# Performance work log

Measured on AMD Instinct MI355X. Metric: run time of the kernel, lower is better.

The kernel has to match this reference:

```python
import jax, jax.numpy as jnp
import numpy as np

N_HEAD = 16
N_EMBD = 1024
B, T = 2, 2048


def setup_inputs() -> dict:
    key = jax.random.key(0)
    ks = jax.random.split(key, 5)
    C = N_EMBD
    x = jax.random.normal(ks[0], (B, T, C), dtype=jnp.float32)
    # nn.Linear default init scale ~ 1/sqrt(fan_in); use small normal for numerics
    s = 1.0 / np.sqrt(C)
    W_attn = jax.random.normal(ks[1], (C, 3 * C), dtype=jnp.float32) * s
    b_attn = jax.random.normal(ks[2], (3 * C,), dtype=jnp.float32) * s
    W_proj = jax.random.normal(ks[3], (C, C), dtype=jnp.float32) * s
    b_proj = jax.random.normal(ks[4], (C,), dtype=jnp.float32) * s
    return {"x": x, "W_attn": W_attn, "b_attn": b_attn, "W_proj": W_proj, "b_proj": b_proj}


def reference(x, W_attn, b_attn, W_proj, b_proj):
    Bs, Ts, C = x.shape
    H = N_HEAD
    D = C // H  # head dim
    qkv = x @ W_attn + b_attn  # [B, T, 3C]
    q, k, v = jnp.split(qkv, 3, axis=2)
    # [B, T, H, D] -> [B, H, T, D]
    q = q.reshape(Bs, Ts, H, D).transpose(0, 2, 1, 3)
    k = k.reshape(Bs, Ts, H, D).transpose(0, 2, 1, 3)
    v = v.reshape(Bs, Ts, H, D).transpose(0, 2, 1, 3)
    scale = 1.0 / jnp.sqrt(jnp.asarray(D, dtype=x.dtype))
    att = jnp.einsum("bhqd,bhkd->bhqk", q, k) * scale  # [B, H, T, T]
    causal = jnp.tril(jnp.ones((Ts, Ts), dtype=bool))
    att = jnp.where(causal, att, -jnp.inf)
    att = jax.nn.softmax(att, axis=-1)
    y = jnp.einsum("bhqk,bhkd->bhqd", att, v)  # [B, H, T, D]
    y = y.transpose(0, 2, 1, 3).reshape(Bs, Ts, C)
    return y @ W_proj + b_proj
```

## Files before the change

kernel.cpp:

```cpp
#include <hip/hip_runtime.h>
#include <stdint.h>

typedef unsigned short u16;
typedef __attribute__((ext_vector_type(8))) short bf16x8;
typedef __attribute__((ext_vector_type(4))) float f32x4;
typedef __attribute__((ext_vector_type(4))) int   i32x4;
typedef __attribute__((ext_vector_type(4))) unsigned int u32x4;
typedef __attribute__((ext_vector_type(4))) unsigned short u16x4;

#define MFMA16(a, b, c) __builtin_amdgcn_mfma_f32_16x16x32_bf16((a), (b), (c), 0, 0, 0)

#define BATCH 2
#define TSEQ  2048
#define CEMB  1024
#define NHEAD 16
#define DHEAD 64
#define BHTOT 32
#define MROWS 4096

__device__ __forceinline__ u16 bf16r(float f) {
  uint32_t u = __builtin_bit_cast(uint32_t, f);
  u += 0x7fffu + ((u >> 16) & 1u);
  return (u16)(u >> 16);
}

__device__ __forceinline__ uint32_t cvt_pk_bf16(float lo, float hi) {
  uint32_t r;
  asm("v_cvt_pk_bf16_f32 %0, %1, %2" : "=v"(r) : "v"(lo), "v"(hi));
  return r;
}

__device__ __forceinline__ float bf2f(short v) {
  return __builtin_bit_cast(float, ((uint32_t)(u16)v) << 16);
}

__device__ __forceinline__ bf16x8 scale8(bf16x8 a, float s) {
  bf16x8 r;
#pragma unroll
  for (int i = 0; i < 8; i++) r[i] = (short)bf16r(bf2f(a[i]) * s);
  return r;
}

__device__ __forceinline__ void gl2lds16(const void* g, void* l) {
  __builtin_amdgcn_global_load_lds(
      (const __attribute__((address_space(1))) uint32_t*)g,
      (__attribute__((address_space(3))) uint32_t*)l, 16, 0, 0);
}

__global__ void prep(const float* __restrict__ x, u16* __restrict__ xb,
                     const float* __restrict__ W_attn, u16* __restrict__ WaT,
                     const float* __restrict__ W_proj, u16* __restrict__ WpT) {
  __shared__ float t[32][33];
  const int bid = blockIdx.x;
  if (bid < 4096) {
    int i = (bid * 256 + threadIdx.x) * 4;
    f32x4 v = *(const f32x4*)(x + i);
    u16x4 o;
    o[0] = bf16r(v[0]); o[1] = bf16r(v[1]); o[2] = bf16r(v[2]); o[3] = bf16r(v[3]);
    *(u16x4*)(xb + i) = o;
    return;
  }
  const float* W; u16* WT; int K, N, idx;
  if (bid < 7168) { W = W_attn; WT = WaT; K = 1024; N = 3072; idx = bid - 4096;
                    idx = (idx % 96) | ((idx / 96) << 16); }
  else            { W = W_proj; WT = WpT; K = 1024; N = 1024; idx = bid - 7168;
                    idx = (idx % 32) | ((idx / 32) << 16); }
  int n0 = (idx & 0xffff) * 32, k0 = (idx >> 16) * 32;
  int tx = threadIdx.x & 31, ty = threadIdx.x >> 5;
  for (int i = 0; i < 4; i++)
    t[ty + i * 8][tx] = W[(size_t)(k0 + ty + i * 8) * N + n0 + tx];
  __syncthreads();
  for (int i = 0; i < 4; i++)
    WT[(size_t)(n0 + ty + i * 8) * K + k0 + tx] = bf16r(t[tx][ty + i * 8]);
}

__device__ __forceinline__ void gemm_mainloop(const u16* __restrict__ A,
                                              const u16* __restrict__ Bt,
                                              int K, int m0, int n0,
                                              u16* AsU, u16* BsU, f32x4 acc[4][4]) {
  const int tid = threadIdx.x;
  const int wv = tid >> 6, ln = tid & 63;
  const int lr = ln & 15, lg = ln >> 4;
  const int wr = (wv >> 1) * 64, wc = (wv & 1) * 64;

  for (int mi = 0; mi < 4; mi++)
    for (int ni = 0; ni < 4; ni++) acc[mi][ni] = f32x4{0.f, 0.f, 0.f, 0.f};

  for (int k0 = 0; k0 < K; k0 += 32) {
    for (int p = 0; p < 2; ++p) {
      int chunk = p * 256 + tid;
      int row = chunk >> 2;
      int c8  = (chunk & 3) << 3;
      u16* abase = AsU + (size_t)(p * 256 + wv * 64) * 8;
      u16* bbase = BsU + (size_t)(p * 256 + wv * 64) * 8;
      gl2lds16(A  + (size_t)(m0 + row) * K + k0 + c8, abase);
      gl2lds16(Bt + (size_t)(n0 + row) * K + k0 + c8, bbase);
    }
    __syncthreads();
    bf16x8 af[4], bf[4];
    for (int mi = 0; mi < 4; mi++)
      af[mi] = *(const bf16x8*)&AsU[(size_t)(wr + mi * 16 + lr) * 32 + lg * 8];
    for (int ni = 0; ni < 4; ni++)
      bf[ni] = *(const bf16x8*)&BsU[(size_t)(wc + ni * 16 + lr) * 32 + lg * 8];
    for (int mi = 0; mi < 4; mi++)
      for (int ni = 0; ni < 4; ni++)
        acc[mi][ni] = MFMA16(af[mi], bf[ni], acc[mi][ni]);
    __syncthreads();
  }
}

__global__ __launch_bounds__(256, 2) void qkv_gemm(const u16* __restrict__ xb,
                                                   const u16* __restrict__ WaT,
                                                   const float* __restrict__ b_attn,
                                                   u16* __restrict__ qb, u16* __restrict__ kb,
                                                   u16* __restrict__ vT) {
  __shared__ u16 AsU[128 * 32];
  __shared__ u16 BsU[128 * 32];
  const int m0 = blockIdx.y * 128, n0 = blockIdx.x * 128;
  f32x4 acc[4][4];
  gemm_mainloop(xb, WaT, CEMB, m0, n0, AsU, BsU, acc);

  const int tid = threadIdx.x;
  const int wv = tid >> 6, ln = tid & 63, lr = ln & 15, lg = ln >> 4;
  const int wr = (wv >> 1) * 64, wc = (wv & 1) * 64;
  for (int mi = 0; mi < 4; mi++)
    for (int ni = 0; ni < 4; ni++) {
      int col = n0 + wc + ni * 16 + lr;
      float bias = b_attn[col];
      int which = col >> 10;
      int cl = col & 1023, h = cl >> 6, d = cl & 63;
      for (int j = 0; j < 4; j++) {
        int m = m0 + wr + mi * 16 + lg * 4 + j;
        int b = m >> 11, t = m & 2047;
        u16 bv = bf16r(acc[mi][ni][j] + bias);
        size_t bh = (size_t)(b * NHEAD + h);
        if (which == 0)      qb[(bh * TSEQ + t) * DHEAD + d] = bv;
        else if (which == 1) kb[(bh * TSEQ + t) * DHEAD + d] = bv;
        else                 vT[(bh * DHEAD + d) * TSEQ + t] = bv;
      }
    }
}

__global__ __launch_bounds__(256, 4) void attn(const u16* __restrict__ qb,
                                               const u16* __restrict__ kb,
                                               const u16* __restrict__ vT,
                                               u16* __restrict__ yb) {
  const int flat = blockIdx.x;
  const int x = flat & 7;
  const int l = flat >> 3;
  const int r = l & 31, a = l >> 5, rq = r & 7;
  const int bh = 4 * x + (r >> 3);
  const int qblk = (a == 0) ? 31 - rq : (a == 1) ? rq : (a == 2) ? 23 - rq : 8 + rq;

  const int tid = threadIdx.x, wv = tid >> 6, ln = tid & 63, lr = ln & 15, lg = ln >> 4;
  const int b1 = lg >> 1, b0 = lg & 1;

  __shared__ u16 Ks[2][64][72];
  __shared__ u16 Vs[2][64][72];

  const int wq0 = qblk * 64 + wv * 16;
  const float SCL = 0.125f * 1.44269504f;

  bf16x8 qf0, qf1;
  {
    const u16* qrow = qb + ((size_t)bh * TSEQ + (wq0 + lr)) * DHEAD + lg * 8;
    qf0 = scale8(*(const bf16x8*)(qrow), SCL);
    qf1 = scale8(*(const bf16x8*)(qrow + 32), SCL);
  }

  f32x4 acc[4];
#pragma unroll
  for (int df = 0; df < 4; df++) acc[df] = f32x4{0.f, 0.f, 0.f, 0.f};
  float mrun = -1e30f, lrun = 0.f;

  const int ntiles = qblk + 1;
  const int srow = tid >> 3, sc8 = (tid & 7) << 3;

  i32x4 kreg[2], vreg[2];
#pragma unroll
  for (int p = 0; p < 2; p++) {
    int row = p * 32 + srow;
    *(i32x4*)&Ks[0][row][sc8] = *(const i32x4*)(kb + ((size_t)bh * TSEQ + row) * DHEAD + sc8);
    *(i32x4*)&Vs[0][row][sc8] = *(const i32x4*)(vT + ((size_t)bh * DHEAD + row) * TSEQ + sc8);
  }
#pragma unroll
  for (int p = 0; p < 2; p++) {
    int row = p * 32 + srow;
    kreg[p] = *(const i32x4*)(kb + ((size_t)bh * TSEQ + 64 + row) * DHEAD + sc8);
    vreg[p] = *(const i32x4*)(vT + ((size_t)bh * DHEAD + row) * TSEQ + 64 + sc8);
  }

  int c = 0;
  for (int kt = 0; kt < ntiles; kt++) {
    const int kbase = kt * 64;
    __syncthreads();

    f32x4 s[4];
#pragma unroll
    for (int st = 0; st < 4; st++) {
      bf16x8 kf0 = *(const bf16x8*)&Ks[c][st * 16 + lr][lg * 8];
      bf16x8 kf1 = *(const bf16x8*)&Ks[c][st * 16 + lr][32 + lg * 8];
      f32x4 z = f32x4{0.f, 0.f, 0.f, 0.f};
      z = MFMA16(kf0, qf0, z);
      z = MFMA16(kf1, qf1, z);
      s[st] = z;
    }

    if (kt + 1 < ntiles) {
#pragma unroll
      for (int p = 0; p < 2; p++) {
        int row = p * 32 + srow;
        *(i32x4*)&Ks[c ^ 1][row][sc8] = kreg[p];
        *(i32x4*)&Vs[c ^ 1][row][sc8] = vreg[p];
      }
    }
    if (kt + 2 < ntiles) {
      const int nb = kbase + 128;
#pragma unroll
      for (int p = 0; p < 2; p++) {
        int row = p * 32 + srow;
        kreg[p] = *(const i32x4*)(kb + ((size_t)bh * TSEQ + nb + row) * DHEAD + sc8);
        vreg[p] = *(const i32x4*)(vT + ((size_t)bh * DHEAD + row) * TSEQ + nb + sc8);
      }
    }

    float mt = -1e30f;
    if (kt == ntiles - 1) {
      const int qg = wq0 + lr;
#pragma unroll
      for (int st = 0; st < 4; st++)
#pragma unroll
        for (int j = 0; j < 4; j++) {
          int kg = kbase + st * 16 + lg * 4 + j;
          float v = (kg <= qg) ? s[st][j] : -1e30f;
          s[st][j] = v;
          mt = fmaxf(mt, v);
        }
    } else {
#pragma unroll
      for (int st = 0; st < 4; st++)
#pragma unroll
        for (int j = 0; j < 4; j++) mt = fmaxf(mt, s[st][j]);
    }
    mt = fmaxf(mt, __shfl_xor(mt, 16));
    mt = fmaxf(mt, __shfl_xor(mt, 32));
    if (!__all(mt <= mrun)) {
      float mnew = fmaxf(mrun, mt);
      float al = __builtin_amdgcn_exp2f(mrun - mnew);
#pragma unroll
      for (int df = 0; df < 4; df++)
#pragma unroll
        for (int j = 0; j < 4; j++) acc[df][j] *= al;
      lrun *= al;
      mrun = mnew;
    }
    float rs = 0.f;
#pragma unroll
    for (int st = 0; st < 4; st++)
#pragma unroll
      for (int j = 0; j < 4; j++) {
        float p = __builtin_amdgcn_exp2f(s[st][j] - mrun);
        s[st][j] = p;
        rs += p;
      }
    rs += __shfl_xor(rs, 16);
    rs += __shfl_xor(rs, 32);
    lrun += rs;

    uint32_t W[4][2];
#pragma unroll
    for (int st = 0; st < 4; st++) {
      W[st][0] = cvt_pk_bf16(s[st][0], s[st][1]);
      W[st][1] = cvt_pk_bf16(s[st][2], s[st][3]);
    }
    uint32_t Ka[2], Kb[2], Xa[2], Xb[2];
#pragma unroll
    for (int h = 0; h < 2; h++) {
      uint32_t S1a = b1 ? W[0][h] : W[1][h];
      uint32_t S1b = b1 ? W[2][h] : W[3][h];
      Xa[h] = __shfl_xor(S1a, 32);
      Xb[h] = __shfl_xor(S1b, 32);
      Ka[h] = b1 ? W[1][h] : W[0][h];
      Kb[h] = b1 ? W[3][h] : W[2][h];
    }
    const bool e = (b0 == b1);
    uint32_t Ta[2], Tb[2], Ra[2], Rb[2];
#pragma unroll
    for (int h = 0; h < 2; h++) {
      uint32_t Cah = e ? Xa[h] : Ka[h];
      uint32_t Cbh = e ? Xb[h] : Kb[h];
      Ta[h] = e ? Ka[h] : Xa[h];
      Tb[h] = e ? Kb[h] : Xb[h];
      Ra[h] = __shfl_xor(Cah, 16);
      Rb[h] = __shfl_xor(Cbh, 16);
    }
    u32x4 w0, w1;
    w0[0] = b0 ? Ra[0] : Ta[0];  w0[1] = b0 ? Ra[1] : Ta[1];
    w0[2] = b0 ? Ta[0] : Ra[0];  w0[3] = b0 ? Ta[1] : Ra[1];
    w1[0] = b0 ? Rb[0] : Tb[0];  w1[1] = b0 ? Rb[1] : Tb[1];
    w1[2] = b0 ? Tb[0] : Rb[0];  w1[3] = b0 ? Tb[1] : Rb[1];
    bf16x8 pf0 = __builtin_bit_cast(bf16x8, w0);
    bf16x8 pf1 = __builtin_bit_cast(bf16x8, w1);

#pragma unroll
    for (int df = 0; df < 4; df++) {
      bf16x8 vf0 = *(const bf16x8*)&Vs[c][df * 16 + lr][lg * 8];
      bf16x8 vf1 = *(const bf16x8*)&Vs[c][df * 16 + lr][32 + lg * 8];
      acc[df] = MFMA16(vf0, pf0, acc[df]);
      acc[df] = MFMA16(vf1, pf1, acc[df]);
    }
    c ^= 1;
  }

  const int b = bh >> 4, h = bh & 15;
  float inv = 1.f / lrun;
  int tg = wq0 + lr;
#pragma unroll
  for (int df = 0; df < 4; df++) {
    u16x4 o;
#pragma unroll
    for (int j = 0; j < 4; j++) o[j] = bf16r(acc[df][j] * inv);
    *(u16x4*)&yb[((size_t)b * TSEQ + tg) * CEMB + h * 64 + df * 16 + lg * 4] = o;
  }
}

__global__ __launch_bounds__(256, 2) void proj_gemm(const u16* __restrict__ yb,
                                                    const u16* __restrict__ WpT,
                                                    const float* __restrict__ b_proj,
                                                    float* __restrict__ out) {
  __shared__ u16 AsU[128 * 32];
  __shared__ u16 BsU[128 * 32];
  const int m0 = blockIdx.y * 128, n0 = blockIdx.x * 128;
  f32x4 acc[4][4];
  gemm_mainloop(yb, WpT, CEMB, m0, n0, AsU, BsU, acc);

  const int tid = threadIdx.x;
  const int wv = tid >> 6, ln = tid & 63, lr = ln & 15, lg = ln >> 4;
  const int wr = (wv >> 1) * 64, wc = (wv & 1) * 64;
  for (int mi = 0; mi < 4; mi++)
    for (int ni = 0; ni < 4; ni++) {
      int col = n0 + wc + ni * 16 + lr;
      float bias = b_proj[col];
      for (int j = 0; j < 4; j++) {
        int m = m0 + wr + mi * 16 + lg * 4 + j;
        out[(size_t)m * CEMB + col] = acc[mi][ni][j] + bias;
      }
    }
}

extern "C" void kernel_launch(void* const* d_in, const int* in_sizes, int n_in,
                              void* d_out, int out_size, void* d_ws, size_t ws_size,
                              hipStream_t stream) {
  const float* x      = (const float*)d_in[0];
  const float* W_attn = (const float*)d_in[1];
  const float* b_attn = (const float*)d_in[2];
  const float* W_proj = (const float*)d_in[3];
  const float* b_proj = (const float*)d_in[4];
  float* out = (float*)d_out;
  char* ws = (char*)d_ws;

  u16* xb  = (u16*)(ws);
  u16* WaT = (u16*)(ws + 8388608);
  u16* WpT = (u16*)(ws + 14680064);
  u16* qb  = (u16*)(ws + 16777216);
  u16* kb  = (u16*)(ws + 25165824);
  u16* vT  = (u16*)(ws + 33554432);
  u16* yb  = (u16*)(ws + 41943040);

  hipLaunchKernelGGL(prep, dim3(8192), dim3(256), 0, stream, x, xb, W_attn, WaT, W_proj, WpT);
  hipLaunchKernelGGL(qkv_gemm, dim3(24, 32), dim3(256), 0, stream, xb, WaT, b_attn, qb, kb, vT);
  hipLaunchKernelGGL(attn, dim3(1024), dim3(256), 0, stream, qb, kb, vT, yb);
  hipLaunchKernelGGL(proj_gemm, dim3(8, 32), dim3(256), 0, stream, yb, WpT, b_proj, out);
}
```

Before: 183.2 us.

## Double-buffer LDS in GEMM mainloop and vectorize V-transpose epilogue stores

The shared GEMM mainloop now uses two LDS buffers, issuing global-to-LDS loads for the next K tile before computing on the current one, so load latency can overlap MFMA work. LDS per block doubles to 32 KB in the QKV and projection GEMMs. The QKV epilogue also packs the four consecutive-t values for the transposed V output into one 8-byte store instead of four scalar stores. A single barrier per iteration is relied on to separate buffer reuse, which depends on the async load ordering being correct.

```diff
diff --git a/kernel.cpp b/kernel.cpp
--- a/kernel.cpp
+++ b/kernel.cpp
@@ -86,26 +86,37 @@
   for (int mi = 0; mi < 4; mi++)
     for (int ni = 0; ni < 4; ni++) acc[mi][ni] = f32x4{0.f, 0.f, 0.f, 0.f};
 
-  for (int k0 = 0; k0 < K; k0 += 32) {
+  auto stage = [&](int buf, int k0) {
+#pragma unroll
     for (int p = 0; p < 2; ++p) {
       int chunk = p * 256 + tid;
       int row = chunk >> 2;
       int c8  = (chunk & 3) << 3;
-      u16* abase = AsU + (size_t)(p * 256 + wv * 64) * 8;
-      u16* bbase = BsU + (size_t)(p * 256 + wv * 64) * 8;
+      u16* abase = AsU + buf * 4096 + (size_t)(p * 256 + wv * 64) * 8;
+      u16* bbase = BsU + buf * 4096 + (size_t)(p * 256 + wv * 64) * 8;
       gl2lds16(A  + (size_t)(m0 + row) * K + k0 + c8, abase);
       gl2lds16(Bt + (size_t)(n0 + row) * K + k0 + c8, bbase);
     }
-    __syncthreads();
+  };
+
+  stage(0, 0);
+  __syncthreads();
+  const int nt = K / 32;
+  int cur = 0;
+  for (int t = 0; t < nt; ++t) {
+    if (t + 1 < nt) stage(cur ^ 1, (t + 1) * 32);
+    const u16* Ab = AsU + cur * 4096;
+    const u16* Bb = BsU + cur * 4096;
     bf16x8 af[4], bf[4];
     for (int mi = 0; mi < 4; mi++)
-      af[mi] = *(const bf16x8*)&AsU[(size_t)(wr + mi * 16 + lr) * 32 + lg * 8];
+      af[mi] = *(const bf16x8*)&Ab[(size_t)(wr + mi * 16 + lr) * 32 + lg * 8];
     for (int ni = 0; ni < 4; ni++)
-      bf[ni] = *(const bf16x8*)&BsU[(size_t)(wc + ni * 16 + lr) * 32 + lg * 8];
+      bf[ni] = *(const bf16x8*)&Bb[(size_t)(wc + ni * 16 + lr) * 32 + lg * 8];
     for (int mi = 0; mi < 4; mi++)
       for (int ni = 0; ni < 4; ni++)
         acc[mi][ni] = MFMA16(af[mi], bf[ni], acc[mi][ni]);
     __syncthreads();
+    cur ^= 1;
   }
 }
 
@@ -114,8 +125,8 @@
                                                    const float* __restrict__ b_attn,
                                                    u16* __restrict__ qb, u16* __restrict__ kb,
                                                    u16* __restrict__ vT) {
-  __shared__ u16 AsU[128 * 32];
-  __shared__ u16 BsU[128 * 32];
+  __shared__ u16 AsU[2 * 128 * 32];
+  __shared__ u16 BsU[2 * 128 * 32];
   const int m0 = blockIdx.y * 128, n0 = blockIdx.x * 128;
   f32x4 acc[4][4];
   gemm_mainloop(xb, WaT, CEMB, m0, n0, AsU, BsU, acc);
@@ -129,14 +140,17 @@
       float bias = b_attn[col];
       int which = col >> 10;
       int cl = col & 1023, h = cl >> 6, d = cl & 63;
-      for (int j = 0; j < 4; j++) {
-        int m = m0 + wr + mi * 16 + lg * 4 + j;
-        int b = m >> 11, t = m & 2047;
-        u16 bv = bf16r(acc[mi][ni][j] + bias);
-        size_t bh = (size_t)(b * NHEAD + h);
-        if (which == 0)      qb[(bh * TSEQ + t) * DHEAD + d] = bv;
-        else if (which == 1) kb[(bh * TSEQ + t) * DHEAD + d] = bv;
-        else                 vT[(bh * DHEAD + d) * TSEQ + t] = bv;
+      int mbase = m0 + wr + mi * 16 + lg * 4;
+      int b = mbase >> 11, t = mbase & 2047;
+      size_t bh = (size_t)(b * NHEAD + h);
+      if (which == 2) {
+        u16x4 o;
+        for (int j = 0; j < 4; j++) o[j] = bf16r(acc[mi][ni][j] + bias);
+        *(u16x4*)&vT[(bh * DHEAD + d) * TSEQ + t] = o;
+      } else {
+        u16* dst = (which == 0) ? qb : kb;
+        for (int j = 0; j < 4; j++)
+          dst[(bh * TSEQ + t + j) * DHEAD + d] = bf16r(acc[mi][ni][j] + bias);
       }
     }
 }
@@ -328,8 +342,8 @@
                                                     const u16* __restrict__ WpT,
                                                     const float* __restrict__ b_proj,
                                                     float* __restrict__ out) {
-  __shared__ u16 AsU[128 * 32];
-  __shared__ u16 BsU[128 * 32];
+  __shared__ u16 AsU[2 * 128 * 32];
+  __shared__ u16 BsU[2 * 128 * 32];
   const int m0 = blockIdx.y * 128, n0 = blockIdx.x * 128;
   f32x4 acc[4][4];
   gemm_mainloop(yb, WpT, CEMB, m0, n0, AsU, BsU, acc);
```

After: 181.4 us. Within noise of the previous version (-1.0%).
